# Kernel tuning notes

Measured on AMD Instinct MI355X. Metric: run time of the kernel, lower is better.

## Reference

```python
import jax, jax.numpy as jnp
import numpy as np

N_FEATURES = 256
D_TOKEN = 512
BATCH = 2048
EPS = 1e-5  # torch LayerNorm default


def setup_inputs() -> dict:
    key = jax.random.key(0)
    k1, k2, k3, k4 = jax.random.split(key, 4)
    values = jax.random.normal(k1, (BATCH, N_FEATURES), dtype=jnp.float32)
    masks = jax.random.uniform(k2, (BATCH, N_FEATURES), dtype=jnp.float32)
    # per-feature Linear(2, d_token): weights stacked as (n_features, 2, d_token)
    bound = 1.0 / np.sqrt(2.0)  # torch Linear init bound for in_features=2
    W = jax.random.uniform(k3, (N_FEATURES, 2, D_TOKEN), dtype=jnp.float32,
                           minval=-bound, maxval=bound)
    b = jax.random.uniform(k4, (N_FEATURES, D_TOKEN), dtype=jnp.float32,
                           minval=-bound, maxval=bound)
    gamma = jnp.ones((D_TOKEN,), dtype=jnp.float32)
    beta = jnp.zeros((D_TOKEN,), dtype=jnp.float32)
    return {"values": values, "masks": masks, "W": W, "b": b,
            "gamma": gamma, "beta": beta}


def reference(values, masks, W, b, gamma, beta):
    # (B, F, 2): stack value and mask per feature (matches torch.stack dim=1 per feature)
    x = jnp.stack([values, masks], axis=-1)
    # batched tiny GEMM over features: one fused einsum instead of F separate Linears
    tokens = jnp.einsum('bfi,fid->bfd', x, W) + b  # (B, F, D)
    # LayerNorm over last dim
    mu = jnp.mean(tokens, axis=-1, keepdims=True)
    var = jnp.var(tokens, axis=-1, keepdims=True)
    normed = (tokens - mu) * jax.lax.rsqrt(var + EPS)
    return normed * gamma + beta
```

## Files before the change

### kernel.cpp

```cpp
#include <hip/hip_runtime.h>

#define BATCH 2048
#define NFEAT 256
#define DTOK  512
#define EPS   1e-5f

typedef float fx4 __attribute__((ext_vector_type(4)));

__global__ __launch_bounds__(256) void FeatureTokenizer_kernel(
    const float* __restrict__ values,
    const float* __restrict__ masks,
    const float* __restrict__ W,
    const float* __restrict__ bias,
    const float* __restrict__ gamma,
    const float* __restrict__ beta,
    float* __restrict__ out)
{
    const int lane = threadIdx.x & 63;
    const int wv   = threadIdx.x >> 6;
    const long long row = (long long)blockIdx.x * 4 + wv;
    const int f  = (int)(row & (NFEAT - 1));
    const int bi = (int)(row >> 8);

    const float v = values[bi * NFEAT + f];
    const float m = masks[bi * NFEAT + f];

    const int dA = lane * 4;
    const int dB = dA + 256;

    const float* w0base = W + ((size_t)f * 2 + 0) * DTOK;
    const float* w1base = W + ((size_t)f * 2 + 1) * DTOK;
    const float* bbase  = bias + (size_t)f * DTOK;

    fx4 w0a = *(const fx4*)(w0base + dA);
    fx4 w0b = *(const fx4*)(w0base + dB);
    fx4 w1a = *(const fx4*)(w1base + dA);
    fx4 w1b = *(const fx4*)(w1base + dB);
    fx4 ba  = *(const fx4*)(bbase  + dA);
    fx4 bb  = *(const fx4*)(bbase  + dB);

    float t[8];
#pragma unroll
    for (int j = 0; j < 4; ++j) {
        t[j]     = fmaf(v, w0a[j], fmaf(m, w1a[j], ba[j]));
        t[j + 4] = fmaf(v, w0b[j], fmaf(m, w1b[j], bb[j]));
    }

    float s = 0.0f, ss = 0.0f;
#pragma unroll
    for (int j = 0; j < 8; ++j) {
        s  += t[j];
        ss += t[j] * t[j];
    }

#pragma unroll
    for (int off = 1; off < 64; off <<= 1) {
        s  += __shfl_xor(s,  off, 64);
        ss += __shfl_xor(ss, off, 64);
    }

    const float mu   = s * (1.0f / DTOK);
    const float var  = ss * (1.0f / DTOK) - mu * mu;
    const float rstd = rsqrtf(var + EPS);

    fx4 ga = *(const fx4*)(gamma + dA);
    fx4 gb = *(const fx4*)(gamma + dB);
    fx4 ea = *(const fx4*)(beta  + dA);
    fx4 eb = *(const fx4*)(beta  + dB);

    fx4 oA, oB;
#pragma unroll
    for (int j = 0; j < 4; ++j) {
        oA[j] = fmaf((t[j]     - mu) * rstd, ga[j], ea[j]);
        oB[j] = fmaf((t[j + 4] - mu) * rstd, gb[j], eb[j]);
    }

    float* orow = out + (size_t)row * DTOK;
    __builtin_nontemporal_store(oA, (fx4*)(orow + dA));
    __builtin_nontemporal_store(oB, (fx4*)(orow + dB));
}

extern "C" void kernel_launch(void* const* d_in, const int* in_sizes, int n_in,
                              void* d_out, int out_size, void* d_ws, size_t ws_size,
                              hipStream_t stream) {
    const float* values = (const float*)d_in[0];
    const float* masks  = (const float*)d_in[1];
    const float* W      = (const float*)d_in[2];
    const float* bias   = (const float*)d_in[3];
    const float* gamma  = (const float*)d_in[4];
    const float* beta   = (const float*)d_in[5];
    float* out = (float*)d_out;

    const long long rows = (long long)BATCH * NFEAT;
    const int blocks = (int)(rows / 4);

    FeatureTokenizer_kernel<<<blocks, 256, 0, stream>>>(
        values, masks, W, bias, gamma, beta, out);
}
```

Measured before the change: 243.8 us.

## Reuse per-feature weights across a chunk of batch rows per wave

Each wave now handles one feature for 16 batch rows, loading W, bias, gamma and beta into registers once. Values and masks are fetched with one coalesced-ish load per lane and then broadcast by shuffle. This cuts redundant weight loads and grows the work per wave, with 16x fewer blocks. The kernel is dominated by output writes (about 268 MB), so the reduction in reads may only shave L2 traffic. The serial loop per wave may also reduce memory-level parallelism.

```diff
diff --git a/kernel.cpp b/kernel.cpp
--- a/kernel.cpp
+++ b/kernel.cpp
@@ -1,9 +1,10 @@
 #include <hip/hip_runtime.h>
 
-#define BATCH 2048
-#define NFEAT 256
-#define DTOK  512
-#define EPS   1e-5f
+#define BATCH  2048
+#define NFEAT  256
+#define DTOK   512
+#define EPS    1e-5f
+#define BCHUNK 16
 
 typedef float fx4 __attribute__((ext_vector_type(4)));
 
@@ -18,12 +19,11 @@
 {
     const int lane = threadIdx.x & 63;
     const int wv   = threadIdx.x >> 6;
-    const long long row = (long long)blockIdx.x * 4 + wv;
-    const int f  = (int)(row & (NFEAT - 1));
-    const int bi = (int)(row >> 8);
-
-    const float v = values[bi * NFEAT + f];
-    const float m = masks[bi * NFEAT + f];
+    const int bid  = blockIdx.x;
+    const int fg   = bid & 63;
+    const int bc   = bid >> 6;
+    const int f    = fg * 4 + wv;
+    const int b0   = bc * BCHUNK;
 
     const int dA = lane * 4;
     const int dB = dA + 256;
@@ -32,52 +32,61 @@
     const float* w1base = W + ((size_t)f * 2 + 1) * DTOK;
     const float* bbase  = bias + (size_t)f * DTOK;
 
-    fx4 w0a = *(const fx4*)(w0base + dA);
-    fx4 w0b = *(const fx4*)(w0base + dB);
-    fx4 w1a = *(const fx4*)(w1base + dA);
-    fx4 w1b = *(const fx4*)(w1base + dB);
-    fx4 ba  = *(const fx4*)(bbase  + dA);
-    fx4 bb  = *(const fx4*)(bbase  + dB);
+    const fx4 w0a = *(const fx4*)(w0base + dA);
+    const fx4 w0b = *(const fx4*)(w0base + dB);
+    const fx4 w1a = *(const fx4*)(w1base + dA);
+    const fx4 w1b = *(const fx4*)(w1base + dB);
+    const fx4 ba  = *(const fx4*)(bbase  + dA);
+    const fx4 bb  = *(const fx4*)(bbase  + dB);
+    const fx4 ga  = *(const fx4*)(gamma + dA);
+    const fx4 gb  = *(const fx4*)(gamma + dB);
+    const fx4 ea  = *(const fx4*)(beta  + dA);
+    const fx4 eb  = *(const fx4*)(beta  + dB);
 
-    float t[8];
-#pragma unroll
-    for (int j = 0; j < 4; ++j) {
-        t[j]     = fmaf(v, w0a[j], fmaf(m, w1a[j], ba[j]));
-        t[j + 4] = fmaf(v, w0b[j], fmaf(m, w1b[j], bb[j]));
+    float vv = 0.0f, mm = 0.0f;
+    if (lane < BCHUNK) {
+        vv = values[(size_t)(b0 + lane) * NFEAT + f];
+        mm = masks [(size_t)(b0 + lane) * NFEAT + f];
     }
 
-    float s = 0.0f, ss = 0.0f;
+    for (int i = 0; i < BCHUNK; ++i) {
+        const float v = __shfl(vv, i, 64);
+        const float m = __shfl(mm, i, 64);
+
+        float t[8];
 #pragma unroll
-    for (int j = 0; j < 8; ++j) {
-        s  += t[j];
-        ss += t[j] * t[j];
+        for (int j = 0; j < 4; ++j) {
+            t[j]     = fmaf(v, w0a[j], fmaf(m, w1a[j], ba[j]));
+            t[j + 4] = fmaf(v, w0b[j], fmaf(m, w1b[j], bb[j]));
+        }
+
+        float s = 0.0f, ss = 0.0f;
+#pragma unroll
+        for (int j = 0; j < 8; ++j) {
+            s  += t[j];
+            ss += t[j] * t[j];
+        }
+#pragma unroll
+        for (int off = 1; off < 64; off <<= 1) {
+            s  += __shfl_xor(s,  off, 64);
+            ss += __shfl_xor(ss, off, 64);
+        }
+
+        const float mu   = s * (1.0f / DTOK);
+        const float var  = ss * (1.0f / DTOK) - mu * mu;
+        const float rstd = rsqrtf(var + EPS);
+
+        fx4 oA, oB;
+#pragma unroll
+        for (int j = 0; j < 4; ++j) {
+            oA[j] = fmaf((t[j]     - mu) * rstd, ga[j], ea[j]);
+            oB[j] = fmaf((t[j + 4] - mu) * rstd, gb[j], eb[j]);
+        }
+
+        float* orow = out + ((size_t)(b0 + i) * NFEAT + f) * DTOK;
+        __builtin_nontemporal_store(oA, (fx4*)(orow + dA));
+        __builtin_nontemporal_store(oB, (fx4*)(orow + dB));
     }
-
-#pragma unroll
-    for (int off = 1; off < 64; off <<= 1) {
-        s  += __shfl_xor(s,  off, 64);
-        ss += __shfl_xor(ss, off, 64);
-    }
-
-    const float mu   = s * (1.0f / DTOK);
-    const float var  = ss * (1.0f / DTOK) - mu * mu;
-    const float rstd = rsqrtf(var + EPS);
-
-    fx4 ga = *(const fx4*)(gamma + dA);
-    fx4 gb = *(const fx4*)(gamma + dB);
-    fx4 ea = *(const fx4*)(beta  + dA);
-    fx4 eb = *(const fx4*)(beta  + dB);
-
-    fx4 oA, oB;
-#pragma unroll
-    for (int j = 0; j < 4; ++j) {
-        oA[j] = fmaf((t[j]     - mu) * rstd, ga[j], ea[j]);
-        oB[j] = fmaf((t[j + 4] - mu) * rstd, gb[j], eb[j]);
-    }
-
-    float* orow = out + (size_t)row * DTOK;
-    __builtin_nontemporal_store(oA, (fx4*)(orow + dA));
-    __builtin_nontemporal_store(oB, (fx4*)(orow + dB));
 }
 
 extern "C" void kernel_launch(void* const* d_in, const int* in_sizes, int n_in,
@@ -91,9 +100,7 @@
     const float* beta   = (const float*)d_in[5];
     float* out = (float*)d_out;
 
-    const long long rows = (long long)BATCH * NFEAT;
-    const int blocks = (int)(rows / 4);
-
+    const int blocks = 64 * (BATCH / BCHUNK);
     FeatureTokenizer_kernel<<<blocks, 256, 0, stream>>>(
         values, masks, W, bias, gamma, beta, out);
 }
```

After: 209.0 us. -14.3%, faster.
